# Optimization experiments

Measured on AMD Instinct MI355X. Metric: run time of the kernel, lower is better.

## Reference

```python
import jax, jax.numpy as jnp
import numpy as np

USER_NUM = 100000
ITEM_NUM = 50000
E = 128   # embedding_size
A = 64    # attention_size
M = 8     # memory_size
B = 4096  # batch
NF = 50   # friends per user


def _l2norm(x, axis):
    # torch F.normalize(p=2): x / max(||x||, eps)
    n = jnp.sqrt(jnp.sum(x * x, axis=axis, keepdims=True))
    return x / jnp.maximum(n, 1e-12)


def setup_inputs() -> dict:
    key = jax.random.key(0)
    ks = jax.random.split(key, 9)
    u = lambda k, shape: jax.random.uniform(k, shape, jnp.float32, -0.1, 0.1)
    return {
        "input_u": jax.random.randint(ks[0], (B,), 0, USER_NUM),
        "input_i": jax.random.randint(ks[1], (B,), 0, ITEM_NUM),
        "input_uf": jax.random.randint(ks[2], (B, NF), 0, USER_NUM + 1),
        "uidW": u(ks[3], (USER_NUM + 1, E)),
        "iidW": u(ks[4], (ITEM_NUM, E)),
        "i_bias": jnp.zeros((ITEM_NUM,), jnp.float32),
        "Key": u(ks[5], (E, M)),
        "Mem": jnp.ones((M, E), jnp.float32),
        "WA": u(ks[6], (E, A)),
        "BA": jnp.zeros((A,), jnp.float32),
        "U_omega": u(ks[7], (A, 1)),
    }


def reference(input_u, input_i, input_uf, uidW, iidW, i_bias, Key, Mem, WA, BA, U_omega):
    user_num = uidW.shape[0] - 1  # padding id
    uid = uidW[input_u]                      # [B, E]
    iid = iidW[input_i]                      # [B, E]
    i_b = i_bias[input_i]                    # [B]
    fe = uidW[input_uf]                      # [B, F, E] friend embeddings
    fn = (input_uf != user_num).astype(uid.dtype)  # [B, F] valid-friend mask

    fe = fn[:, :, None] * fe
    uid_n = _l2norm(uid, axis=1)
    fe_n = _l2norm(fe, axis=2)
    cross = uid_n[:, None, :] * fe_n                     # [B, F, E]
    att_key = jnp.einsum('bfe,em->bfm', cross, Key)      # [B, F, M]
    att_mem = jax.nn.softmax(att_key, axis=0)            # softmax over batch (faithful to dim=0)
    att_mem = fn[:, :, None] * att_mem
    f1 = jnp.einsum('bfm,me->bfe', att_mem, Mem)         # [B, F, E]
    f2 = f1 * fe
    h = jax.nn.relu(jnp.einsum('bfe,ea->bfa', f2, WA) + BA)
    j = jnp.exp(jnp.einsum('bfa,ao->bfo', h, U_omega))   # [B, F, 1]
    j = fn[:, :, None] * j
    w = j / (jnp.sum(j, axis=1, keepdims=True) + 1e-8)
    friend = jnp.sum(w * f2, axis=1)                     # [B, E] (dropout p=0 -> identity)
    user = uid + friend
    score = jnp.sum(user * iid, axis=1) + i_b            # [B]
    return score
```

## Files before the change

kernel.cpp:

```cpp
#include <hip/hip_runtime.h>

#define EDIM 128
#define MDIM 8
#define ADIM 64
#define NFR  50
#define NCOL (NFR * MDIM)

typedef __attribute__((ext_vector_type(8))) short short8;
typedef __attribute__((ext_vector_type(4))) float f32x4;

__device__ __forceinline__ float waveReduceSum(float v) {
    #pragma unroll
    for (int s = 32; s >= 1; s >>= 1) v += __shfl_xor(v, s, 64);
    return v;
}
__device__ __forceinline__ short f2bf(float x) {
    unsigned u = __float_as_uint(x);
    u += 0x7FFFu + ((u >> 16) & 1u);
    return (short)(u >> 16);
}
__device__ __forceinline__ float bf2f(short s) {
    return __uint_as_float(((unsigned)(unsigned short)s) << 16);
}
__device__ __forceinline__ int fragIdx(int r, int e) {
    return ((((r >> 4) << 2) | (e >> 5)) * 64 + ((e >> 3) & 3) * 16 + (r & 15)) * 8 + (e & 7);
}

__global__ __launch_bounds__(256)
void k0_prep(const float* __restrict__ WA, const float* __restrict__ Key,
             short* __restrict__ WAfrag, short* __restrict__ Keyfrag)
{
    int t = blockIdx.x * 256 + threadIdx.x;
    if (t < 1024) {
        int lane = t & 63;
        int Kt = (t >> 6) & 3;
        int Nt = t >> 8;
        int n  = Nt * 16 + (lane & 15);
        int k0 = Kt * 32 + (lane >> 4) * 8;
        short8 v;
        #pragma unroll
        for (int j = 0; j < 8; ++j) v[j] = f2bf(WA[(size_t)(k0 + j) * ADIM + n]);
        *(short8*)(WAfrag + (size_t)t * 8) = v;
    } else if (t < 1280) {
        int i = t - 1024;
        int lane = i & 63;
        int Kt = i >> 6;
        int n  = lane & 15;
        int k0 = Kt * 32 + (lane >> 4) * 8;
        short8 v;
        #pragma unroll
        for (int j = 0; j < 8; ++j)
            v[j] = (n < MDIM) ? f2bf(Key[(size_t)(k0 + j) * MDIM + n]) : (short)0;
        *(short8*)(Keyfrag + (size_t)i * 8) = v;
    }
}

__global__ __launch_bounds__(256, 4)
void k1_attkey(const int* __restrict__ input_u, const int* __restrict__ input_uf,
               const float* __restrict__ uidW, const short* __restrict__ Keyfrag,
               float* __restrict__ att_key, int user_num)
{
    const int b = blockIdx.x, t = threadIdx.x, w = t >> 6, l = t & 63;
    __shared__ short crossF[64 * EDIM];

    const int u = input_u[b];
    float u0 = uidW[(size_t)u * EDIM + l];
    float u1 = uidW[(size_t)u * EDIM + 64 + l];
    float ss = waveReduceSum(u0 * u0 + u1 * u1);
    float uinv = 1.0f / fmaxf(sqrtf(ss), 1e-12f);
    u0 *= uinv; u1 *= uinv;

    const int* uf = input_uf + (size_t)b * NFR;
    #pragma unroll 2
    for (int f = w; f < NFR; f += 4) {
        const int fid = uf[f];
        const float fn = (fid != user_num) ? 1.0f : 0.0f;
        float e0 = uidW[(size_t)fid * EDIM + l] * fn;
        float e1 = uidW[(size_t)fid * EDIM + 64 + l] * fn;
        float fss = waveReduceSum(e0 * e0 + e1 * e1);
        float finv = 1.0f / fmaxf(sqrtf(fss), 1e-12f);
        crossF[fragIdx(f, l)]      = f2bf(u0 * (e0 * finv));
        crossF[fragIdx(f, l + 64)] = f2bf(u1 * (e1 * finv));
    }
    __syncthreads();

    f32x4 acc = {0.f, 0.f, 0.f, 0.f};
    #pragma unroll
    for (int Kt = 0; Kt < 4; ++Kt) {
        short8 a  = *(const short8*)&crossF[(((w << 2) | Kt) * 64 + l) * 8];
        short8 bf = *(const short8*)(Keyfrag + (size_t)((Kt * 64 + l)) * 8);
        acc = __builtin_amdgcn_mfma_f32_16x16x32_bf16(a, bf, acc, 0, 0, 0);
    }
    const int m = l & 15;
    if (m < MDIM) {
        const int fbase = w * 16 + (l >> 4) * 4;
        #pragma unroll
        for (int r = 0; r < 4; ++r) {
            int f = fbase + r;
            if (f < NFR) att_key[((size_t)b * NFR + f) * MDIM + m] = acc[r];
        }
    }
}

__global__ __launch_bounds__(256)
void k2a_stats(const float* __restrict__ ak,
               float* __restrict__ Pm, float* __restrict__ Ps, int B)
{
    const int cg = blockIdx.x;
    const int rc = blockIdx.y;
    const int t = threadIdx.x;
    const int c = t & 15, r = t >> 4;
    const int col = cg * 16 + c;
    const int base = rc * (B >> 4);

    float x[16];
    #pragma unroll
    for (int k = 0; k < 16; ++k)
        x[k] = ak[(size_t)(base + k * 16 + r) * NCOL + col];
    float m = x[0];
    #pragma unroll
    for (int k = 1; k < 16; ++k) m = fmaxf(m, x[k]);
    float s = 0.f;
    #pragma unroll
    for (int k = 0; k < 16; ++k) s += __expf(x[k] - m);

    __shared__ float mL[16][17], sL[16][17];
    mL[r][c] = m; sL[r][c] = s;
    __syncthreads();
    if (t < 16) {
        float M = mL[0][t];
        #pragma unroll
        for (int rr = 1; rr < 16; ++rr) M = fmaxf(M, mL[rr][t]);
        float S = 0.f;
        #pragma unroll
        for (int rr = 0; rr < 16; ++rr) S += sL[rr][t] * __expf(mL[rr][t] - M);
        Pm[rc * NCOL + cg * 16 + t] = M;
        Ps[rc * NCOL + cg * 16 + t] = S;
    }
}

__global__ __launch_bounds__(512)
void k2b_merge(const float* __restrict__ Pm, const float* __restrict__ Ps,
               float* __restrict__ mx, float* __restrict__ ise)
{
    int col = threadIdx.x;
    if (col >= NCOL) return;
    float M = -3.4e38f;
    #pragma unroll
    for (int rc = 0; rc < 16; ++rc) M = fmaxf(M, Pm[rc * NCOL + col]);
    float S = 0.f;
    #pragma unroll
    for (int rc = 0; rc < 16; ++rc) S += Ps[rc * NCOL + col] * __expf(Pm[rc * NCOL + col] - M);
    mx[col] = M;
    ise[col] = 1.0f / S;
}

__global__ __launch_bounds__(256, 4)
void k3_final(const int* __restrict__ input_u, const int* __restrict__ input_i,
              const int* __restrict__ input_uf, const float* __restrict__ uidW,
              const float* __restrict__ iidW, const float* __restrict__ i_bias,
              const float* __restrict__ Mem, const short* __restrict__ WAfrag,
              const float* __restrict__ BA, const float* __restrict__ U_omega,
              const float* __restrict__ att_key, const float* __restrict__ mx,
              const float* __restrict__ ise, float* __restrict__ out,
              int user_num)
{
    const int b = blockIdx.x, t = threadIdx.x, w = t >> 6, l = t & 63;
    __shared__ short f2b[64 * EDIM];
    __shared__ float mxL[NCOL], iseL[NCOL];
    __shared__ float pPart[4 * 64];
    __shared__ float jL[64];
    __shared__ float accL[4][EDIM];
    __shared__ float red2[2];
    __shared__ float wsS;

    for (int i = t; i < NCOL; i += 256) { mxL[i] = mx[i]; iseL[i] = ise[i]; }

    float mem0[MDIM], mem1[MDIM];
    #pragma unroll
    for (int m = 0; m < MDIM; ++m) {
        mem0[m] = Mem[m * EDIM + l];
        mem1[m] = Mem[m * EDIM + 64 + l];
    }
    __syncthreads();

    const int* uf = input_uf + (size_t)b * NFR;

    #pragma unroll 2
    for (int f = w; f < NFR; f += 4) {
        const int fid = uf[f];
        const float fn = (fid != user_num) ? 1.0f : 0.0f;
        float fe0 = uidW[(size_t)fid * EDIM + l] * fn;
        float fe1 = uidW[(size_t)fid * EDIM + 64 + l] * fn;
        const float* ak = att_key + ((size_t)b * NFR + f) * MDIM;
        float f10 = 0.f, f11 = 0.f;
        #pragma unroll
        for (int m = 0; m < MDIM; ++m) {
            float a = fn * __expf(ak[m] - mxL[f * MDIM + m]) * iseL[f * MDIM + m];
            f10 += a * mem0[m];
            f11 += a * mem1[m];
        }
        f2b[fragIdx(f, l)]      = f2bf(f10 * fe0);
        f2b[fragIdx(f, l + 64)] = f2bf(f11 * fe1);
    }
    __syncthreads();

    f32x4 acc[4];
    #pragma unroll
    for (int Mt = 0; Mt < 4; ++Mt) acc[Mt] = (f32x4){0.f, 0.f, 0.f, 0.f};
    #pragma unroll
    for (int Kt = 0; Kt < 4; ++Kt) {
        short8 bf = *(const short8*)(WAfrag + (size_t)(((w << 2) | Kt) * 64 + l) * 8);
        #pragma unroll
        for (int Mt = 0; Mt < 4; ++Mt) {
            short8 a = *(const short8*)&f2b[(((Mt << 2) | Kt) * 64 + l) * 8];
            acc[Mt] = __builtin_amdgcn_mfma_f32_16x16x32_bf16(a, bf, acc[Mt], 0, 0, 0);
        }
    }

    const int aIdx = w * 16 + (l & 15);
    const float ba = BA[aIdx];
    const float uo = U_omega[aIdx];
    float v[16];
    #pragma unroll
    for (int Mt = 0; Mt < 4; ++Mt)
        #pragma unroll
        for (int r = 0; r < 4; ++r)
            v[Mt * 4 + r] = fmaxf(acc[Mt][r] + ba, 0.f) * uo;

    const bool c0 = l & 1, c1 = l & 2, c2 = l & 4, c3 = l & 8;
    #pragma unroll
    for (int k = 0; k < 8; ++k) {
        float lo = v[k], hi = v[k + 8];
        float send = c0 ? lo : hi;
        float recv = __shfl_xor(send, 1, 64);
        v[k] = c0 ? (hi + recv) : (lo + recv);
    }
    #pragma unroll
    for (int k = 0; k < 4; ++k) {
        float lo = v[k], hi = v[k + 4];
        float send = c1 ? lo : hi;
        float recv = __shfl_xor(send, 2, 64);
        v[k] = c1 ? (hi + recv) : (lo + recv);
    }
    #pragma unroll
    for (int k = 0; k < 2; ++k) {
        float lo = v[k], hi = v[k + 2];
        float send = c2 ? lo : hi;
        float recv = __shfl_xor(send, 4, 64);
        v[k] = c2 ? (hi + recv) : (lo + recv);
    }
    {
        float lo = v[0], hi = v[1];
        float send = c3 ? lo : hi;
        float recv = __shfl_xor(send, 8, 64);
        v[0] = c3 ? (hi + recv) : (lo + recv);
    }
    const int vIdx = ((l & 1) << 3) | ((l & 2) << 1) | ((l & 4) >> 1) | ((l & 8) >> 3);
    const int fLane = (vIdx >> 2) * 16 + (l >> 4) * 4 + (vIdx & 3);
    pPart[w * 64 + fLane] = v[0];
    __syncthreads();

    if (t < 64) {
        float p = pPart[t] + pPart[64 + t] + pPart[128 + t] + pPart[192 + t];
        float jv = 0.f;
        if (t < NFR && uf[t] != user_num) jv = __expf(p);
        jL[t] = jv;
        float wsum = waveReduceSum(jv);
        if (t == 0) wsS = wsum + 1e-8f;
    }
    __syncthreads();

    {
        const int fbeg = w * 13;
        const int fend = min(NFR, fbeg + 13);
        float a0 = 0.f, a1 = 0.f;
        for (int f = fbeg; f < fend; ++f) {
            float jf = jL[f];
            a0 += jf * bf2f(f2b[fragIdx(f, l)]);
            a1 += jf * bf2f(f2b[fragIdx(f, l + 64)]);
        }
        accL[w][l] = a0; accL[w][64 + l] = a1;
    }
    __syncthreads();

    if (t < EDIM) {
        const float winv = 1.0f / wsS;
        float fr = (accL[0][t] + accL[1][t] + accL[2][t] + accL[3][t]) * winv;
        const int u = input_u[b];
        const int ii = input_i[b];
        float sc = (uidW[(size_t)u * EDIM + t] + fr) * iidW[(size_t)ii * EDIM + t];
        float p = waveReduceSum(sc);
        if ((t & 63) == 0) red2[t >> 6] = p;
    }
    __syncthreads();
    if (t == 0) out[b] = red2[0] + red2[1] + i_bias[input_i[b]];
}

extern "C" void kernel_launch(void* const* d_in, const int* in_sizes, int n_in,
                              void* d_out, int out_size, void* d_ws, size_t ws_size,
                              hipStream_t stream)
{
    const int*   input_u  = (const int*)d_in[0];
    const int*   input_i  = (const int*)d_in[1];
    const int*   input_uf = (const int*)d_in[2];
    const float* uidW     = (const float*)d_in[3];
    const float* iidW     = (const float*)d_in[4];
    const float* i_bias   = (const float*)d_in[5];
    const float* Key      = (const float*)d_in[6];
    const float* Mem      = (const float*)d_in[7];
    const float* WA       = (const float*)d_in[8];
    const float* BA       = (const float*)d_in[9];
    const float* U_om     = (const float*)d_in[10];

    const int B = in_sizes[0];
    const int user_num = in_sizes[3] / EDIM - 1;

    float* att = (float*)d_ws;
    float* Pm  = att + (size_t)B * NCOL;
    float* Ps  = Pm + 16 * NCOL;
    float* mx  = Ps + 16 * NCOL;
    float* ise = mx + NCOL;
    short* WAfrag  = (short*)(ise + NCOL);
    short* Keyfrag = WAfrag + 4 * 4 * 64 * 8;

    k0_prep<<<5, 256, 0, stream>>>(WA, Key, WAfrag, Keyfrag);
    k1_attkey<<<B, 256, 0, stream>>>(input_u, input_uf, uidW, Keyfrag, att, user_num);
    k2a_stats<<<dim3(25, 16), 256, 0, stream>>>(att, Pm, Ps, B);
    k2b_merge<<<1, 512, 0, stream>>>(Pm, Ps, mx, ise);
    k3_final<<<B, 256, 0, stream>>>(input_u, input_i, input_uf, uidW, iidW, i_bias,
                                    Mem, WAfrag, BA, U_om, att, mx, ise,
                                    (float*)d_out, user_num);
}
```

Before: 194.6 us.

## Vectorize friend gathers and swizzle LDS fragment layout in attkey and final kernels

```diff
diff --git a/kernel.cpp b/kernel.cpp
--- a/kernel.cpp
+++ b/kernel.cpp
@@ -22,9 +22,13 @@
 __device__ __forceinline__ float bf2f(short s) {
     return __uint_as_float(((unsigned)(unsigned short)s) << 16);
 }
-__device__ __forceinline__ int fragIdx(int r, int e) {
-    return ((((r >> 4) << 2) | (e >> 5)) * 64 + ((e >> 3) & 3) * 16 + (r & 15)) * 8 + (e & 7);
-}
+__device__ __forceinline__ int fragOff(int r, int e) {
+    int q = (e >> 3) & 3;
+    int slot = (q * 16 + (r & 15)) ^ (q << 1);
+    int block = ((r >> 4) << 2) | (e >> 5);
+    return (block * 64 + slot) * 8;
+}
+__device__ __forceinline__ int slotR(int l) { return l ^ (((l >> 4) & 3) << 1); }
 
 __global__ __launch_bounds__(256)
 void k0_prep(const float* __restrict__ WA, const float* __restrict__ Key,
@@ -62,32 +66,63 @@
 {
     const int b = blockIdx.x, t = threadIdx.x, w = t >> 6, l = t & 63;
     __shared__ short crossF[64 * EDIM];
+    __shared__ float uidnL[EDIM];
+    __shared__ float redW[4];
+    __shared__ int ufL[64];
 
     const int u = input_u[b];
-    float u0 = uidW[(size_t)u * EDIM + l];
-    float u1 = uidW[(size_t)u * EDIM + 64 + l];
-    float ss = waveReduceSum(u0 * u0 + u1 * u1);
-    float uinv = 1.0f / fmaxf(sqrtf(ss), 1e-12f);
-    u0 *= uinv; u1 *= uinv;
-
-    const int* uf = input_uf + (size_t)b * NFR;
-    #pragma unroll 2
-    for (int f = w; f < NFR; f += 4) {
-        const int fid = uf[f];
-        const float fn = (fid != user_num) ? 1.0f : 0.0f;
-        float e0 = uidW[(size_t)fid * EDIM + l] * fn;
-        float e1 = uidW[(size_t)fid * EDIM + 64 + l] * fn;
-        float fss = waveReduceSum(e0 * e0 + e1 * e1);
-        float finv = 1.0f / fmaxf(sqrtf(fss), 1e-12f);
-        crossF[fragIdx(f, l)]      = f2bf(u0 * (e0 * finv));
-        crossF[fragIdx(f, l + 64)] = f2bf(u1 * (e1 * finv));
+    float x = (t < EDIM) ? uidW[(size_t)u * EDIM + t] : 0.f;
+    float s = waveReduceSum(x * x);
+    if (l == 0) redW[w] = s;
+    if (t < NFR) ufL[t] = input_uf[(size_t)b * NFR + t];
+    else if (t < 64) ufL[t] = user_num;
+    __syncthreads();
+    float uinv = 1.0f / fmaxf(sqrtf(redW[0] + redW[1] + redW[2] + redW[3]), 1e-12f);
+    if (t < EDIM) uidnL[t] = x * uinv;
+    __syncthreads();
+
+    const int kg = t & 15, fl = t >> 4;
+    const int e0 = kg * 8;
+    float4 un0 = *(const float4*)&uidnL[e0];
+    float4 un1 = *(const float4*)&uidnL[e0 + 4];
+
+    #pragma unroll
+    for (int it = 0; it < 4; ++it) {
+        int f = fl + 16 * it;
+        short8 outv = {0, 0, 0, 0, 0, 0, 0, 0};
+        if (f < NFR) {
+            int fid = ufL[f];
+            float fn = (fid != user_num) ? 1.f : 0.f;
+            const float* fp = uidW + (size_t)fid * EDIM + e0;
+            float4 g0 = *(const float4*)fp;
+            float4 g1 = *(const float4*)(fp + 4);
+            g0.x *= fn; g0.y *= fn; g0.z *= fn; g0.w *= fn;
+            g1.x *= fn; g1.y *= fn; g1.z *= fn; g1.w *= fn;
+            float fss = g0.x*g0.x + g0.y*g0.y + g0.z*g0.z + g0.w*g0.w
+                      + g1.x*g1.x + g1.y*g1.y + g1.z*g1.z + g1.w*g1.w;
+            fss += __shfl_xor(fss, 1, 64);
+            fss += __shfl_xor(fss, 2, 64);
+            fss += __shfl_xor(fss, 4, 64);
+            fss += __shfl_xor(fss, 8, 64);
+            float inv = 1.0f / fmaxf(sqrtf(fss), 1e-12f);
+            outv[0] = f2bf(un0.x * g0.x * inv);
+            outv[1] = f2bf(un0.y * g0.y * inv);
+            outv[2] = f2bf(un0.z * g0.z * inv);
+            outv[3] = f2bf(un0.w * g0.w * inv);
+            outv[4] = f2bf(un1.x * g1.x * inv);
+            outv[5] = f2bf(un1.y * g1.y * inv);
+            outv[6] = f2bf(un1.z * g1.z * inv);
+            outv[7] = f2bf(un1.w * g1.w * inv);
+        }
+        *(short8*)&crossF[fragOff(f, e0)] = outv;
     }
     __syncthreads();
 
     f32x4 acc = {0.f, 0.f, 0.f, 0.f};
+    const int sl = slotR(l);
     #pragma unroll
     for (int Kt = 0; Kt < 4; ++Kt) {
-        short8 a  = *(const short8*)&crossF[(((w << 2) | Kt) * 64 + l) * 8];
+        short8 a  = *(const short8*)&crossF[(((w << 2) | Kt) * 64 + sl) * 8];
         short8 bf = *(const short8*)(Keyfrag + (size_t)((Kt * 64 + l)) * 8);
         acc = __builtin_amdgcn_mfma_f32_16x16x32_bf16(a, bf, acc, 0, 0, 0);
     }
@@ -166,45 +201,73 @@
               int user_num)
 {
     const int b = blockIdx.x, t = threadIdx.x, w = t >> 6, l = t & 63;
-    __shared__ short f2b[64 * EDIM];
-    __shared__ float mxL[NCOL], iseL[NCOL];
+    __shared__ short f2F[64 * EDIM];
+    __shared__ float amL[NCOL];
+    __shared__ int ufL[64];
     __shared__ float pPart[4 * 64];
-    __shared__ float jL[64];
-    __shared__ float accL[4][EDIM];
+    __shared__ float jxL[64];
+    __shared__ float accW[4][EDIM];
     __shared__ float red2[2];
     __shared__ float wsS;
 
-    for (int i = t; i < NCOL; i += 256) { mxL[i] = mx[i]; iseL[i] = ise[i]; }
-
-    float mem0[MDIM], mem1[MDIM];
+    if (t < NFR) ufL[t] = input_uf[(size_t)b * NFR + t];
+    else if (t < 64) ufL[t] = user_num;
+    __syncthreads();
+
+    for (int i = t; i < NCOL; i += 256) {
+        float ak = att_key[(size_t)b * NCOL + i];
+        amL[i] = (ufL[i >> 3] != user_num) ? __expf(ak - mx[i]) * ise[i] : 0.f;
+    }
+
+    const int kg = t & 15, fl = t >> 4;
+    const int e0 = kg * 8;
+    float4 mA[MDIM], mB[MDIM];
     #pragma unroll
     for (int m = 0; m < MDIM; ++m) {
-        mem0[m] = Mem[m * EDIM + l];
-        mem1[m] = Mem[m * EDIM + 64 + l];
-    }
-    __syncthreads();
-
-    const int* uf = input_uf + (size_t)b * NFR;
-
-    #pragma unroll 2
-    for (int f = w; f < NFR; f += 4) {
-        const int fid = uf[f];
-        const float fn = (fid != user_num) ? 1.0f : 0.0f;
-        float fe0 = uidW[(size_t)fid * EDIM + l] * fn;
-        float fe1 = uidW[(size_t)fid * EDIM + 64 + l] * fn;
-        const float* ak = att_key + ((size_t)b * NFR + f) * MDIM;
-        float f10 = 0.f, f11 = 0.f;
-        #pragma unroll
-        for (int m = 0; m < MDIM; ++m) {
-            float a = fn * __expf(ak[m] - mxL[f * MDIM + m]) * iseL[f * MDIM + m];
-            f10 += a * mem0[m];
-            f11 += a * mem1[m];
+        mA[m] = *(const float4*)&Mem[m * EDIM + e0];
+        mB[m] = *(const float4*)&Mem[m * EDIM + e0 + 4];
+    }
+    __syncthreads();
+
+    #pragma unroll
+    for (int it = 0; it < 4; ++it) {
+        int f = fl + 16 * it;
+        short8 outv = {0, 0, 0, 0, 0, 0, 0, 0};
+        if (f < NFR) {
+            int fid = ufL[f];
+            float fn = (fid != user_num) ? 1.f : 0.f;
+            const float* fp = uidW + (size_t)fid * EDIM + e0;
+            float4 g0 = *(const float4*)fp;
+            float4 g1 = *(const float4*)(fp + 4);
+            float4 am0 = *(const float4*)&amL[f * 8];
+            float4 am1 = *(const float4*)&amL[f * 8 + 4];
+            float4 fa = {0.f, 0.f, 0.f, 0.f}, fb = {0.f, 0.f, 0.f, 0.f};
+            #pragma unroll
+            for (int m = 0; m < 4; ++m) {
+                float c0 = (&am0.x)[m], c1 = (&am1.x)[m];
+                fa.x += c0 * mA[m].x + c1 * mA[m + 4].x;
+                fa.y += c0 * mA[m].y + c1 * mA[m + 4].y;
+                fa.z += c0 * mA[m].z + c1 * mA[m + 4].z;
+                fa.w += c0 * mA[m].w + c1 * mA[m + 4].w;
+                fb.x += c0 * mB[m].x + c1 * mB[m + 4].x;
+                fb.y += c0 * mB[m].y + c1 * mB[m + 4].y;
+                fb.z += c0 * mB[m].z + c1 * mB[m + 4].z;
+                fb.w += c0 * mB[m].w + c1 * mB[m + 4].w;
+            }
+            outv[0] = f2bf(fa.x * g0.x * fn);
+            outv[1] = f2bf(fa.y * g0.y * fn);
+            outv[2] = f2bf(fa.z * g0.z * fn);
+            outv[3] = f2bf(fa.w * g0.w * fn);
+            outv[4] = f2bf(fb.x * g1.x * fn);
+            outv[5] = f2bf(fb.y * g1.y * fn);
+            outv[6] = f2bf(fb.z * g1.z * fn);
+            outv[7] = f2bf(fb.w * g1.w * fn);
         }
-        f2b[fragIdx(f, l)]      = f2bf(f10 * fe0);
-        f2b[fragIdx(f, l + 64)] = f2bf(f11 * fe1);
-    }
-    __syncthreads();
-
+        *(short8*)&f2F[fragOff(f, e0)] = outv;
+    }
+    __syncthreads();
+
+    const int sl = slotR(l);
     f32x4 acc[4];
     #pragma unroll
     for (int Mt = 0; Mt < 4; ++Mt) acc[Mt] = (f32x4){0.f, 0.f, 0.f, 0.f};
@@ -213,7 +276,7 @@
         short8 bf = *(const short8*)(WAfrag + (size_t)(((w << 2) | Kt) * 64 + l) * 8);
         #pragma unroll
         for (int Mt = 0; Mt < 4; ++Mt) {
-            short8 a = *(const short8*)&f2b[(((Mt << 2) | Kt) * 64 + l) * 8];
+            short8 a = *(const short8*)&f2F[(((Mt << 2) | Kt) * 64 + sl) * 8];
             acc[Mt] = __builtin_amdgcn_mfma_f32_16x16x32_bf16(a, bf, acc[Mt], 0, 0, 0);
         }
     }
@@ -264,29 +327,36 @@
     if (t < 64) {
         float p = pPart[t] + pPart[64 + t] + pPart[128 + t] + pPart[192 + t];
         float jv = 0.f;
-        if (t < NFR && uf[t] != user_num) jv = __expf(p);
-        jL[t] = jv;
+        if (t < NFR && ufL[t] != user_num) jv = __expf(p);
+        jxL[t] = jv;
         float wsum = waveReduceSum(jv);
         if (t == 0) wsS = wsum + 1e-8f;
     }
     __syncthreads();
 
-    {
-        const int fbeg = w * 13;
-        const int fend = min(NFR, fbeg + 13);
-        float a0 = 0.f, a1 = 0.f;
-        for (int f = fbeg; f < fend; ++f) {
-            float jf = jL[f];
-            a0 += jf * bf2f(f2b[fragIdx(f, l)]);
-            a1 += jf * bf2f(f2b[fragIdx(f, l + 64)]);
-        }
-        accL[w][l] = a0; accL[w][64 + l] = a1;
+    float pa[8] = {0.f, 0.f, 0.f, 0.f, 0.f, 0.f, 0.f, 0.f};
+    #pragma unroll
+    for (int it = 0; it < 4; ++it) {
+        int f = fl + 16 * it;
+        float jf = jxL[f];
+        short8 vv = *(const short8*)&f2F[fragOff(f, e0)];
+        #pragma unroll
+        for (int j = 0; j < 8; ++j) pa[j] += jf * bf2f(vv[j]);
+    }
+    #pragma unroll
+    for (int j = 0; j < 8; ++j) {
+        pa[j] += __shfl_xor(pa[j], 16, 64);
+        pa[j] += __shfl_xor(pa[j], 32, 64);
+    }
+    if (l < 16) {
+        #pragma unroll
+        for (int j = 0; j < 8; ++j) accW[w][l * 8 + j] = pa[j];
     }
     __syncthreads();
 
     if (t < EDIM) {
         const float winv = 1.0f / wsS;
-        float fr = (accL[0][t] + accL[1][t] + accL[2][t] + accL[3][t]) * winv;
+        float fr = (accW[0][t] + accW[1][t] + accW[2][t] + accW[3][t]) * winv;
         const int u = input_u[b];
         const int ii = input_i[b];
         float sc = (uidW[(size_t)u * EDIM + t] + fr) * iidW[(size_t)ii * EDIM + t];
```

Result: faster. 172.7 us (-11.3%).

## Restructure attention kernels: per-lane friend rows, MFMA memory/score products, fused softmax merge

Applied to the files above, without the earlier changes.

```diff
diff --git a/kernel.cpp b/kernel.cpp
--- a/kernel.cpp
+++ b/kernel.cpp
@@ -19,86 +19,109 @@
     u += 0x7FFFu + ((u >> 16) & 1u);
     return (short)(u >> 16);
 }
-__device__ __forceinline__ float bf2f(short s) {
-    return __uint_as_float(((unsigned)(unsigned short)s) << 16);
-}
-__device__ __forceinline__ int fragIdx(int r, int e) {
-    return ((((r >> 4) << 2) | (e >> 5)) * 64 + ((e >> 3) & 3) * 16 + (r & 15)) * 8 + (e & 7);
-}
 
 __global__ __launch_bounds__(256)
-void k0_prep(const float* __restrict__ WA, const float* __restrict__ Key,
-             short* __restrict__ WAfrag, short* __restrict__ Keyfrag)
+void k0_prep(const float* __restrict__ WA, const float* __restrict__ Mem,
+             const float* __restrict__ Key,
+             short* __restrict__ WATf, short* __restrict__ MemTf,
+             short* __restrict__ KeyTf)
 {
     int t = blockIdx.x * 256 + threadIdx.x;
+    int lane = t & 63, c = lane & 15, g = (lane >> 4) & 3;
+    short8 v = {0, 0, 0, 0, 0, 0, 0, 0};
     if (t < 1024) {
-        int lane = t & 63;
-        int Kt = (t >> 6) & 3;
-        int Nt = t >> 8;
-        int n  = Nt * 16 + (lane & 15);
-        int k0 = Kt * 32 + (lane >> 4) * 8;
-        short8 v;
-        #pragma unroll
-        for (int j = 0; j < 8; ++j) v[j] = f2bf(WA[(size_t)(k0 + j) * ADIM + n]);
-        *(short8*)(WAfrag + (size_t)t * 8) = v;
-    } else if (t < 1280) {
-        int i = t - 1024;
-        int lane = i & 63;
-        int Kt = i >> 6;
-        int n  = lane & 15;
-        int k0 = Kt * 32 + (lane >> 4) * 8;
-        short8 v;
-        #pragma unroll
-        for (int j = 0; j < 8; ++j)
-            v[j] = (n < MDIM) ? f2bf(Key[(size_t)(k0 + j) * MDIM + n]) : (short)0;
-        *(short8*)(Keyfrag + (size_t)i * 8) = v;
+        int frag = t >> 6, Ma = frag >> 2, Kt = frag & 3;
+        int a = Ma * 16 + c;
+        #pragma unroll
+        for (int j = 0; j < 8; ++j) {
+            int e = Kt * 32 + g * 8 + j;
+            v[j] = f2bf(WA[(size_t)e * ADIM + a]);
+        }
+        *(short8*)(WATf + (size_t)t * 8) = v;
+    } else if (t < 1536) {
+        int i = t - 1024, Mt = i >> 6;
+        int e = Mt * 16 + c;
+        #pragma unroll
+        for (int j = 0; j < 8; ++j) {
+            int k = g * 8 + j;
+            v[j] = (k < MDIM) ? f2bf(Mem[(size_t)k * EDIM + e]) : (short)0;
+        }
+        *(short8*)(MemTf + (size_t)i * 8) = v;
+    } else if (t < 1792) {
+        int i = t - 1536, Kt = i >> 6;
+        #pragma unroll
+        for (int j = 0; j < 8; ++j) {
+            int e = Kt * 32 + g * 8 + j;
+            v[j] = (c < MDIM) ? f2bf(Key[(size_t)e * MDIM + c]) : (short)0;
+        }
+        *(short8*)(KeyTf + (size_t)i * 8) = v;
     }
 }
 
 __global__ __launch_bounds__(256, 4)
 void k1_attkey(const int* __restrict__ input_u, const int* __restrict__ input_uf,
-               const float* __restrict__ uidW, const short* __restrict__ Keyfrag,
+               const float* __restrict__ uidW, const short* __restrict__ KeyTf,
                float* __restrict__ att_key, int user_num)
 {
     const int b = blockIdx.x, t = threadIdx.x, w = t >> 6, l = t & 63;
-    __shared__ short crossF[64 * EDIM];
-
+    const int c = l & 15, g = l >> 4;
+    __shared__ float uidn[EDIM];
+    __shared__ float redW[4];
+    __shared__ int ufL[64];
+
+    if (t < 64) ufL[t] = (t < NFR) ? input_uf[(size_t)b * NFR + t] : user_num;
     const int u = input_u[b];
-    float u0 = uidW[(size_t)u * EDIM + l];
-    float u1 = uidW[(size_t)u * EDIM + 64 + l];
-    float ss = waveReduceSum(u0 * u0 + u1 * u1);
-    float uinv = 1.0f / fmaxf(sqrtf(ss), 1e-12f);
-    u0 *= uinv; u1 *= uinv;
-
-    const int* uf = input_uf + (size_t)b * NFR;
-    #pragma unroll 2
-    for (int f = w; f < NFR; f += 4) {
-        const int fid = uf[f];
-        const float fn = (fid != user_num) ? 1.0f : 0.0f;
-        float e0 = uidW[(size_t)fid * EDIM + l] * fn;
-        float e1 = uidW[(size_t)fid * EDIM + 64 + l] * fn;
-        float fss = waveReduceSum(e0 * e0 + e1 * e1);
-        float finv = 1.0f / fmaxf(sqrtf(fss), 1e-12f);
-        crossF[fragIdx(f, l)]      = f2bf(u0 * (e0 * finv));
-        crossF[fragIdx(f, l + 64)] = f2bf(u1 * (e1 * finv));
-    }
-    __syncthreads();
+    float x = (t < EDIM) ? uidW[(size_t)u * EDIM + t] : 0.f;
+    float ss = waveReduceSum(x * x);
+    if (l == 0) redW[w] = ss;
+    __syncthreads();
+    float uinv = 1.0f / fmaxf(sqrtf(redW[0] + redW[1] + redW[2] + redW[3]), 1e-12f);
+    if (t < EDIM) uidn[t] = x * uinv;
+    __syncthreads();
+
+    const int f = w * 16 + c;
+    const int fid = ufL[f];
+    const float fn = (f < NFR && fid != user_num) ? 1.0f : 0.0f;
+    const float* fp = uidW + (size_t)fid * EDIM;
+
+    float4 fe[4][2];
+    #pragma unroll
+    for (int Kt = 0; Kt < 4; ++Kt) {
+        fe[Kt][0] = *(const float4*)(fp + Kt * 32 + g * 8);
+        fe[Kt][1] = *(const float4*)(fp + Kt * 32 + g * 8 + 4);
+    }
+    float fss = 0.f;
+    #pragma unroll
+    for (int Kt = 0; Kt < 4; ++Kt)
+        #pragma unroll
+        for (int h = 0; h < 2; ++h) {
+            float4 q = fe[Kt][h];
+            fss += q.x * q.x + q.y * q.y + q.z * q.z + q.w * q.w;
+        }
+    fss += __shfl_xor(fss, 16, 64);
+    fss += __shfl_xor(fss, 32, 64);
+    const float inv2 = fn / fmaxf(sqrtf(fss), 1e-12f);
 
     f32x4 acc = {0.f, 0.f, 0.f, 0.f};
     #pragma unroll
     for (int Kt = 0; Kt < 4; ++Kt) {
-        short8 a  = *(const short8*)&crossF[(((w << 2) | Kt) * 64 + l) * 8];
-        short8 bf = *(const short8*)(Keyfrag + (size_t)((Kt * 64 + l)) * 8);
-        acc = __builtin_amdgcn_mfma_f32_16x16x32_bf16(a, bf, acc, 0, 0, 0);
-    }
-    const int m = l & 15;
-    if (m < MDIM) {
-        const int fbase = w * 16 + (l >> 4) * 4;
-        #pragma unroll
-        for (int r = 0; r < 4; ++r) {
-            int f = fbase + r;
-            if (f < NFR) att_key[((size_t)b * NFR + f) * MDIM + m] = acc[r];
-        }
+        float4 un0 = *(const float4*)&uidn[Kt * 32 + g * 8];
+        float4 un1 = *(const float4*)&uidn[Kt * 32 + g * 8 + 4];
+        short8 bf;
+        bf[0] = f2bf(un0.x * fe[Kt][0].x * inv2);
+        bf[1] = f2bf(un0.y * fe[Kt][0].y * inv2);
+        bf[2] = f2bf(un0.z * fe[Kt][0].z * inv2);
+        bf[3] = f2bf(un0.w * fe[Kt][0].w * inv2);
+        bf[4] = f2bf(un1.x * fe[Kt][1].x * inv2);
+        bf[5] = f2bf(un1.y * fe[Kt][1].y * inv2);
+        bf[6] = f2bf(un1.z * fe[Kt][1].z * inv2);
+        bf[7] = f2bf(un1.w * fe[Kt][1].w * inv2);
+        short8 af = *(const short8*)(KeyTf + (size_t)(Kt * 64 + l) * 8);
+        acc = __builtin_amdgcn_mfma_f32_16x16x32_bf16(af, bf, acc, 0, 0, 0);
+    }
+    if (f < NFR && g < 2) {
+        float4 st = {acc[0], acc[1], acc[2], acc[3]};
+        *(float4*)&att_key[(size_t)b * NCOL + f * MDIM + g * 4] = st;
     }
 }
 
@@ -139,162 +162,157 @@
     }
 }
 
-__global__ __launch_bounds__(512)
-void k2b_merge(const float* __restrict__ Pm, const float* __restrict__ Ps,
-               float* __restrict__ mx, float* __restrict__ ise)
-{
-    int col = threadIdx.x;
-    if (col >= NCOL) return;
-    float M = -3.4e38f;
-    #pragma unroll
-    for (int rc = 0; rc < 16; ++rc) M = fmaxf(M, Pm[rc * NCOL + col]);
-    float S = 0.f;
-    #pragma unroll
-    for (int rc = 0; rc < 16; ++rc) S += Ps[rc * NCOL + col] * __expf(Pm[rc * NCOL + col] - M);
-    mx[col] = M;
-    ise[col] = 1.0f / S;
-}
-
 __global__ __launch_bounds__(256, 4)
 void k3_final(const int* __restrict__ input_u, const int* __restrict__ input_i,
               const int* __restrict__ input_uf, const float* __restrict__ uidW,
               const float* __restrict__ iidW, const float* __restrict__ i_bias,
-              const float* __restrict__ Mem, const short* __restrict__ WAfrag,
+              const short* __restrict__ WATf, const short* __restrict__ MemTf,
               const float* __restrict__ BA, const float* __restrict__ U_omega,
-              const float* __restrict__ att_key, const float* __restrict__ mx,
-              const float* __restrict__ ise, float* __restrict__ out,
-              int user_num)
+              const float* __restrict__ att_key,
+              const float* __restrict__ Pm, const float* __restrict__ Ps,
+              float* __restrict__ out, int user_num)
 {
     const int b = blockIdx.x, t = threadIdx.x, w = t >> 6, l = t & 63;
-    __shared__ short f2b[64 * EDIM];
-    __shared__ float mxL[NCOL], iseL[NCOL];
-    __shared__ float pPart[4 * 64];
-    __shared__ float jL[64];
-    __shared__ float accL[4][EDIM];
-    __shared__ float red2[2];
-    __shared__ float wsS;
-
-    for (int i = t; i < NCOL; i += 256) { mxL[i] = mx[i]; iseL[i] = ise[i]; }
-
-    float mem0[MDIM], mem1[MDIM];
-    #pragma unroll
-    for (int m = 0; m < MDIM; ++m) {
-        mem0[m] = Mem[m * EDIM + l];
-        mem1[m] = Mem[m * EDIM + 64 + l];
-    }
-    __syncthreads();
-
-    const int* uf = input_uf + (size_t)b * NFR;
-
-    #pragma unroll 2
-    for (int f = w; f < NFR; f += 4) {
-        const int fid = uf[f];
-        const float fn = (fid != user_num) ? 1.0f : 0.0f;
-        float fe0 = uidW[(size_t)fid * EDIM + l] * fn;
-        float fe1 = uidW[(size_t)fid * EDIM + 64 + l] * fn;
-        const float* ak = att_key + ((size_t)b * NFR + f) * MDIM;
-        float f10 = 0.f, f11 = 0.f;
-        #pragma unroll
-        for (int m = 0; m < MDIM; ++m) {
-            float a = fn * __expf(ak[m] - mxL[f * MDIM + m]) * iseL[f * MDIM + m];
-            f10 += a * mem0[m];
-            f11 += a * mem1[m];
-        }
-        f2b[fragIdx(f, l)]      = f2bf(f10 * fe0);
-        f2b[fragIdx(f, l + 64)] = f2bf(f11 * fe1);
-    }
-    __syncthreads();
-
-    f32x4 acc[4];
-    #pragma unroll
-    for (int Mt = 0; Mt < 4; ++Mt) acc[Mt] = (f32x4){0.f, 0.f, 0.f, 0.f};
+    const int c = l & 15, g = l >> 4;
+    __shared__ short WATs[16 * 64 * 8];
+    __shared__ short f2s[4][4 * 64 * 8];
+    __shared__ float amL[512];
+    __shared__ float uidL[EDIM], iidL[EDIM];
+    __shared__ float baL[ADIM], uoL[ADIM];
+    __shared__ int ufL[64];
+    __shared__ float sjW[4], syW[4];
+
+    if (t < 64) ufL[t] = (t < NFR) ? input_uf[(size_t)b * NFR + t] : user_num;
+    __syncthreads();
+
+    const int u = input_u[b];
+    const int ii = input_i[b];
+    if (t < EDIM) {
+        uidL[t] = uidW[(size_t)u * EDIM + t];
+        iidL[t] = iidW[(size_t)ii * EDIM + t];
+    }
+    if (t < ADIM) { baL[t] = BA[t]; uoL[t] = U_omega[t]; }
+
+    {
+        const uint4* src = (const uint4*)WATf;
+        uint4* dst = (uint4*)WATs;
+        #pragma unroll
+        for (int i = 0; i < 4; ++i) dst[t + 256 * i] = src[t + 256 * i];
+    }
+
+    const int f = w * 16 + c;
+    const int fid = ufL[f];
+    const float fn = (f < NFR && fid != user_num) ? 1.0f : 0.0f;
+    float4 fe4[8];
+    {
+        const float* fp = uidW + (size_t)fid * EDIM;
+        #pragma unroll
+        for (int Mt = 0; Mt < 8; ++Mt)
+            fe4[Mt] = *(const float4*)(fp + Mt * 16 + g * 4);
+    }
+
+    for (int i = t; i < 512; i += 256) {
+        float amv = 0.f;
+        if (i < NCOL) {
+            float M = -3.4e38f;
+            #pragma unroll
+            for (int rc = 0; rc < 16; ++rc) M = fmaxf(M, Pm[rc * NCOL + i]);
+            float S = 0.f;
+            #pragma unroll
+            for (int rc = 0; rc < 16; ++rc)
+                S += Ps[rc * NCOL + i] * __expf(Pm[rc * NCOL + i] - M);
+            float ak = att_key[(size_t)b * NCOL + i];
+            if (ufL[i >> 3] != user_num) amv = __expf(ak - M) / S;
+        }
+        amL[i] = amv;
+    }
+    __syncthreads();
+
+    short8 amf = {0, 0, 0, 0, 0, 0, 0, 0};
+    if (g == 0) {
+        float4 a0 = *(const float4*)&amL[f * 8];
+        float4 a1 = *(const float4*)&amL[f * 8 + 4];
+        amf[0] = f2bf(a0.x); amf[1] = f2bf(a0.y);
+        amf[2] = f2bf(a0.z); amf[3] = f2bf(a0.w);
+        amf[4] = f2bf(a1.x); amf[5] = f2bf(a1.y);
+        amf[6] = f2bf(a1.z); amf[7] = f2bf(a1.w);
+    }
+
+    f32x4 C1[8];
+    #pragma unroll
+    for (int Mt = 0; Mt < 8; ++Mt) {
+        short8 af = *(const short8*)(MemTf + (size_t)(Mt * 64 + l) * 8);
+        f32x4 z = {0.f, 0.f, 0.f, 0.f};
+        C1[Mt] = __builtin_amdgcn_mfma_f32_16x16x32_bf16(af, amf, z, 0, 0, 0);
+    }
+
+    #pragma unroll
+    for (int Mt = 0; Mt < 8; ++Mt) {
+        float q0 = C1[Mt][0] * fe4[Mt].x * fn;
+        float q1 = C1[Mt][1] * fe4[Mt].y * fn;
+        float q2 = C1[Mt][2] * fe4[Mt].z * fn;
+        float q3 = C1[Mt][3] * fe4[Mt].w * fn;
+        unsigned d0 = ((unsigned)(unsigned short)f2bf(q0)) |
+                      (((unsigned)(unsigned short)f2bf(q1)) << 16);
+        unsigned d1 = ((unsigned)(unsigned short)f2bf(q2)) |
+                      (((unsigned)(unsigned short)f2bf(q3)) << 16);
+        int lane2 = ((Mt & 1) * 2 + (g >> 1)) * 16 + c;
+        int off = ((Mt >> 1) * 64 + lane2) * 8 + (g & 1) * 4;
+        uint2 dd = {d0, d1};
+        *(uint2*)&f2s[w][off] = dd;
+    }
+
+    f32x4 C2[4], C3 = {0.f, 0.f, 0.f, 0.f};
+    #pragma unroll
+    for (int Ma = 0; Ma < 4; ++Ma) C2[Ma] = (f32x4){0.f, 0.f, 0.f, 0.f};
     #pragma unroll
     for (int Kt = 0; Kt < 4; ++Kt) {
-        short8 bf = *(const short8*)(WAfrag + (size_t)(((w << 2) | Kt) * 64 + l) * 8);
-        #pragma unroll
-        for (int Mt = 0; Mt < 4; ++Mt) {
-            short8 a = *(const short8*)&f2b[(((Mt << 2) | Kt) * 64 + l) * 8];
-            acc[Mt] = __builtin_amdgcn_mfma_f32_16x16x32_bf16(a, bf, acc[Mt], 0, 0, 0);
-        }
-    }
-
-    const int aIdx = w * 16 + (l & 15);
-    const float ba = BA[aIdx];
-    const float uo = U_omega[aIdx];
-    float v[16];
-    #pragma unroll
-    for (int Mt = 0; Mt < 4; ++Mt)
-        #pragma unroll
-        for (int r = 0; r < 4; ++r)
-            v[Mt * 4 + r] = fmaxf(acc[Mt][r] + ba, 0.f) * uo;
-
-    const bool c0 = l & 1, c1 = l & 2, c2 = l & 4, c3 = l & 8;
-    #pragma unroll
-    for (int k = 0; k < 8; ++k) {
-        float lo = v[k], hi = v[k + 8];
-        float send = c0 ? lo : hi;
-        float recv = __shfl_xor(send, 1, 64);
-        v[k] = c0 ? (hi + recv) : (lo + recv);
-    }
-    #pragma unroll
-    for (int k = 0; k < 4; ++k) {
-        float lo = v[k], hi = v[k + 4];
-        float send = c1 ? lo : hi;
-        float recv = __shfl_xor(send, 2, 64);
-        v[k] = c1 ? (hi + recv) : (lo + recv);
-    }
-    #pragma unroll
-    for (int k = 0; k < 2; ++k) {
-        float lo = v[k], hi = v[k + 2];
-        float send = c2 ? lo : hi;
-        float recv = __shfl_xor(send, 4, 64);
-        v[k] = c2 ? (hi + recv) : (lo + recv);
-    }
-    {
-        float lo = v[0], hi = v[1];
-        float send = c3 ? lo : hi;
-        float recv = __shfl_xor(send, 8, 64);
-        v[0] = c3 ? (hi + recv) : (lo + recv);
-    }
-    const int vIdx = ((l & 1) << 3) | ((l & 2) << 1) | ((l & 4) >> 1) | ((l & 8) >> 3);
-    const int fLane = (vIdx >> 2) * 16 + (l >> 4) * 4 + (vIdx & 3);
-    pPart[w * 64 + fLane] = v[0];
-    __syncthreads();
-
-    if (t < 64) {
-        float p = pPart[t] + pPart[64 + t] + pPart[128 + t] + pPart[192 + t];
-        float jv = 0.f;
-        if (t < NFR && uf[t] != user_num) jv = __expf(p);
-        jL[t] = jv;
-        float wsum = waveReduceSum(jv);
-        if (t == 0) wsS = wsum + 1e-8f;
-    }
-    __syncthreads();
-
-    {
-        const int fbeg = w * 13;
-        const int fend = min(NFR, fbeg + 13);
-        float a0 = 0.f, a1 = 0.f;
-        for (int f = fbeg; f < fend; ++f) {
-            float jf = jL[f];
-            a0 += jf * bf2f(f2b[fragIdx(f, l)]);
-            a1 += jf * bf2f(f2b[fragIdx(f, l + 64)]);
-        }
-        accL[w][l] = a0; accL[w][64 + l] = a1;
-    }
-    __syncthreads();
-
-    if (t < EDIM) {
-        const float winv = 1.0f / wsS;
-        float fr = (accL[0][t] + accL[1][t] + accL[2][t] + accL[3][t]) * winv;
-        const int u = input_u[b];
-        const int ii = input_i[b];
-        float sc = (uidW[(size_t)u * EDIM + t] + fr) * iidW[(size_t)ii * EDIM + t];
-        float p = waveReduceSum(sc);
-        if ((t & 63) == 0) red2[t >> 6] = p;
-    }
-    __syncthreads();
-    if (t == 0) out[b] = red2[0] + red2[1] + i_bias[input_i[b]];
+        short8 bf = *(const short8*)&f2s[w][(Kt * 64 + l) * 8];
+        #pragma unroll
+        for (int Ma = 0; Ma < 4; ++Ma) {
+            short8 af = *(const short8*)&WATs[((Ma * 4 + Kt) * 64 + l) * 8];
+            C2[Ma] = __builtin_amdgcn_mfma_f32_16x16x32_bf16(af, bf, C2[Ma], 0, 0, 0);
+        }
+        short8 itf = {0, 0, 0, 0, 0, 0, 0, 0};
+        if (c == 0) {
+            float4 i0 = *(const float4*)&iidL[Kt * 32 + g * 8];
+            float4 i1 = *(const float4*)&iidL[Kt * 32 + g * 8 + 4];
+            itf[0] = f2bf(i0.x); itf[1] = f2bf(i0.y);
+            itf[2] = f2bf(i0.z); itf[3] = f2bf(i0.w);
+            itf[4] = f2bf(i1.x); itf[5] = f2bf(i1.y);
+            itf[6] = f2bf(i1.z); itf[7] = f2bf(i1.w);
+        }
+        C3 = __builtin_amdgcn_mfma_f32_16x16x32_bf16(itf, bf, C3, 0, 0, 0);
+    }
+
+    float psum = 0.f;
+    #pragma unroll
+    for (int Ma = 0; Ma < 4; ++Ma) {
+        float4 ba4 = *(const float4*)&baL[Ma * 16 + g * 4];
+        float4 uo4 = *(const float4*)&uoL[Ma * 16 + g * 4];
+        psum += fmaxf(C2[Ma][0] + ba4.x, 0.f) * uo4.x;
+        psum += fmaxf(C2[Ma][1] + ba4.y, 0.f) * uo4.y;
+        psum += fmaxf(C2[Ma][2] + ba4.z, 0.f) * uo4.z;
+        psum += fmaxf(C2[Ma][3] + ba4.w, 0.f) * uo4.w;
+    }
+    psum += __shfl_xor(psum, 16, 64);
+    psum += __shfl_xor(psum, 32, 64);
+    const float jv = (fn > 0.f) ? __expf(psum) : 0.f;
+    const float jy = jv * C3[0];
+    float sj = waveReduceSum((g == 0) ? jv : 0.f);
+    float sy = waveReduceSum(jy);
+    if (l == 0) { sjW[w] = sj; syW[w] = sy; }
+    __syncthreads();
+
+    if (w == 0) {
+        float s = uidL[l] * iidL[l] + uidL[l + 64] * iidL[l + 64];
+        s = waveReduceSum(s);
+        if (l == 0) {
+            float Sj = sjW[0] + sjW[1] + sjW[2] + sjW[3] + 1e-8f;
+            float Sy = syW[0] + syW[1] + syW[2] + syW[3];
+            out[b] = s + Sy / Sj + i_bias[ii];
+        }
+    }
 }
 
 extern "C" void kernel_launch(void* const* d_in, const int* in_sizes, int n_in,
@@ -319,16 +337,14 @@
     float* att = (float*)d_ws;
     float* Pm  = att + (size_t)B * NCOL;
     float* Ps  = Pm + 16 * NCOL;
-    float* mx  = Ps + 16 * NCOL;
-    float* ise = mx + NCOL;
-    short* WAfrag  = (short*)(ise + NCOL);
-    short* Keyfrag = WAfrag + 4 * 4 * 64 * 8;
-
-    k0_prep<<<5, 256, 0, stream>>>(WA, Key, WAfrag, Keyfrag);
-    k1_attkey<<<B, 256, 0, stream>>>(input_u, input_uf, uidW, Keyfrag, att, user_num);
+    short* WATf  = (short*)(Ps + 16 * NCOL);
+    short* MemTf = WATf + 16 * 64 * 8;
+    short* KeyTf = MemTf + 8 * 64 * 8;
+
+    k0_prep<<<7, 256, 0, stream>>>(WA, Mem, Key, WATf, MemTf, KeyTf);
+    k1_attkey<<<B, 256, 0, stream>>>(input_u, input_uf, uidW, KeyTf, att, user_num);
     k2a_stats<<<dim3(25, 16), 256, 0, stream>>>(att, Pm, Ps, B);
-    k2b_merge<<<1, 512, 0, stream>>>(Pm, Ps, mx, ise);
     k3_final<<<B, 256, 0, stream>>>(input_u, input_i, input_uf, uidW, iidW, i_bias,
-                                    Mem, WAfrag, BA, U_om, att, mx, ise,
+                                    WATf, MemTf, BA, U_om, att, Pm, Ps,
                                     (float*)d_out, user_num);
 }
```

After: 175.9 us. 1.11x faster.
